# Performance work log

Hardware: AMD Instinct MI355X
Metric: run time of the kernel (lower is better)

The kernel has to match this reference:

```python
import jax, jax.numpy as jnp
import numpy as np

D_MODEL = 512
N_HEADS = 8
HEAD_DIM = D_MODEL // N_HEADS
BATCH = 2
SEQ = 4096
MAX_SEQ = 4096


def _rope_tables(max_len, dim):
    # freqs = 1/10000^(arange(0,dim,2)/dim); outer(t, freqs); polar -> cos/sin
    inv = 1.0 / (10000.0 ** (np.arange(0, dim, 2, dtype=np.float32) / dim))
    t = np.arange(max_len, dtype=np.float32)
    ang = np.outer(t, inv)  # [max_len, dim/2]
    return jnp.asarray(np.cos(ang)), jnp.asarray(np.sin(ang))


def _apply_rope(x, cos, sin):
    # x: [B, S, H, Hd]; complex-pair rotation over last dim pairs
    B, S, H, Hd = x.shape
    xr = x.reshape(B, S, H, Hd // 2, 2)
    xe, xo = xr[..., 0], xr[..., 1]
    c = cos[:S][None, :, None, :]  # [1,S,1,Hd/2]
    s = sin[:S][None, :, None, :]
    re = xe * c - xo * s
    im = xe * s + xo * c
    return jnp.stack([re, im], axis=-1).reshape(B, S, H, Hd)


def setup_inputs() -> dict:
    key = jax.random.key(0)
    kx, kq, kk, kv, ko = jax.random.split(key, 5)
    std = 1.0 / np.sqrt(D_MODEL)
    return {
        "x": jax.random.normal(kx, (BATCH, SEQ, D_MODEL), dtype=jnp.float32),
        "Wq": jax.random.normal(kq, (D_MODEL, D_MODEL), dtype=jnp.float32) * std,
        "Wk": jax.random.normal(kk, (D_MODEL, D_MODEL), dtype=jnp.float32) * std,
        "Wv": jax.random.normal(kv, (D_MODEL, D_MODEL), dtype=jnp.float32) * std,
        "Wo": jax.random.normal(ko, (D_MODEL, D_MODEL), dtype=jnp.float32) * std,
    }


def reference(x, Wq, Wk, Wv, Wo):
    B, S, D = x.shape
    cos, sin = _rope_tables(MAX_SEQ, HEAD_DIM)
    # nn.Linear: y = x @ W.T
    q = (x @ Wq.T).reshape(B, S, N_HEADS, HEAD_DIM)
    k = (x @ Wk.T).reshape(B, S, N_HEADS, HEAD_DIM)
    v = (x @ Wv.T).reshape(B, S, N_HEADS, HEAD_DIM)
    q = _apply_rope(q, cos, sin)
    k = _apply_rope(k, cos, sin)
    scale = HEAD_DIM ** (-0.5)
    # [B,H,S,S]
    scores = jnp.einsum("bshd,bthd->bhst", q, k) * scale
    causal = jnp.tril(jnp.ones((S, S), dtype=bool))
    scores = jnp.where(causal[None, None], scores, -jnp.inf)
    attn = jax.nn.softmax(scores, axis=-1)
    out = jnp.einsum("bhst,bthd->bshd", attn, v).reshape(B, S, D)
    return out @ Wo.T
```

## Files before the change

### kernel.cpp

```cpp
#include <hip/hip_runtime.h>
#include <hip/hip_bf16.h>
#include <math.h>

#define D_MODEL 512
#define N_HEADS 8
#define HEAD_DIM 64
#define BATCH 2
#define SEQ 4096
#define M_ROWS (BATCH*SEQ)

typedef __attribute__((ext_vector_type(8))) short short8;
typedef __attribute__((ext_vector_type(4))) float f32x4;

__device__ inline short f2bf(float f) {
  union { float f; unsigned u; } v; v.f = f;
  unsigned u = v.u;
  unsigned r = u + 0x7FFFu + ((u >> 16) & 1u);
  return (short)(r >> 16);
}
__device__ inline float bf2f(short s) {
  union { unsigned u; float f; } v; v.u = ((unsigned)(unsigned short)s) << 16;
  return v.f;
}

__device__ inline void gll16(const void* g, void* l) {
  __builtin_amdgcn_global_load_lds(
      (const __attribute__((address_space(1))) unsigned int*)g,
      (__attribute__((address_space(3))) unsigned int*)l, 16, 0, 0);
}

__global__ void prep_kernel(const float* __restrict__ x,
                            const float* __restrict__ Wq,
                            const float* __restrict__ Wk,
                            const float* __restrict__ Wv,
                            const float* __restrict__ Wo,
                            short* __restrict__ xb,
                            short* __restrict__ Wqkv,
                            short* __restrict__ Wob,
                            float* __restrict__ cosT,
                            float* __restrict__ sinT) {
  int i = blockIdx.x * blockDim.x + threadIdx.x;
  if (i < M_ROWS * D_MODEL) xb[i] = f2bf(x[i]);
  if (i < 3 * D_MODEL * D_MODEL) {
    int t = i >> 18;
    int r = i & 262143;
    const float* W = (t == 0) ? Wq : ((t == 1) ? Wk : Wv);
    Wqkv[i] = f2bf(W[r]);
  }
  if (i < D_MODEL * D_MODEL) Wob[i] = f2bf(Wo[i]);
  if (i < SEQ * 32) {
    int s = i >> 5, p = i & 31;
    float e = (float)(2 * p) * (1.0f / 64.0f);
    float inv = powf(10000.0f, -e);
    float ang = (float)s * inv;
    float sv, cv;
    sincosf(ang, &sv, &cv);
    cosT[i] = cv; sinT[i] = sv;
  }
}

template<int MODE>
__global__ __launch_bounds__(256) void gemm_kernel(const short* __restrict__ A,
                                                   const short* __restrict__ B,
                                                   float* __restrict__ out_f,
                                                   short* __restrict__ Qb,
                                                   short* __restrict__ Kb,
                                                   short* __restrict__ Vb,
                                                   const float* __restrict__ cosT,
                                                   const float* __restrict__ sinT) {
  __shared__ short smem[128 * 72 * 2];
  short (*As)[72] = (short(*)[72])smem;
  short (*Bs)[72] = (short(*)[72])(smem + 128 * 72);
  short (*Cs)[136] = (short(*)[136])smem;

  const int m0 = blockIdx.x * 128;
  const int n0 = blockIdx.y * 128;
  const int tid = threadIdx.x;
  const int lane = tid & 63, wid = tid >> 6;
  const int wm = wid >> 1, wn = wid & 1;
  const int l15 = lane & 15, g = lane >> 4;
  const int Kdim = 512;

  f32x4 acc[4][4] = {};

  for (int kt = 0; kt < Kdim; kt += 64) {
    __syncthreads();
    for (int it = 0; it < 4; ++it) {
      int c = it * 256 + tid;
      int row = c >> 3, col = (c & 7) << 3;
      *(short8*)&As[row][col] = *(const short8*)&A[(m0 + row) * Kdim + kt + col];
      *(short8*)&Bs[row][col] = *(const short8*)&B[(n0 + row) * Kdim + kt + col];
    }
    __syncthreads();
    for (int kk = 0; kk < 64; kk += 32) {
      short8 a[4], b[4];
      for (int mi = 0; mi < 4; ++mi)
        a[mi] = *(const short8*)&As[wm * 64 + mi * 16 + l15][kk + (g << 3)];
      for (int ni = 0; ni < 4; ++ni)
        b[ni] = *(const short8*)&Bs[wn * 64 + ni * 16 + l15][kk + (g << 3)];
      for (int mi = 0; mi < 4; ++mi)
        for (int ni = 0; ni < 4; ++ni)
          acc[mi][ni] = __builtin_amdgcn_mfma_f32_16x16x32_bf16(a[mi], b[ni], acc[mi][ni], 0, 0, 0);
    }
  }

  if (MODE == 1) {
    for (int mi = 0; mi < 4; ++mi)
      for (int ni = 0; ni < 4; ++ni)
        for (int r = 0; r < 4; ++r) {
          int row_g = m0 + wm * 64 + mi * 16 + (g << 2) + r;
          int col_g = n0 + wn * 64 + ni * 16 + l15;
          out_f[row_g * 512 + col_g] = acc[mi][ni][r];
        }
    return;
  }

  __syncthreads();
  for (int mi = 0; mi < 4; ++mi)
    for (int ni = 0; ni < 4; ++ni)
      for (int r = 0; r < 4; ++r)
        Cs[wm * 64 + mi * 16 + (g << 2) + r][wn * 64 + ni * 16 + l15] =
            f2bf(acc[mi][ni][r]);
  __syncthreads();

  const int t_blk = n0 >> 9;
  if (t_blk < 2) {
    short* dst = (t_blk == 0) ? Qb : Kb;
    const float qs = (t_blk == 0) ? 0.18033688011112042f : 1.0f;
#pragma unroll
    for (int it = 0; it < 8; ++it) {
      int row = (tid >> 4) + (it << 4);
      int colb = (tid & 15) << 3;
      short8 vv = *(const short8*)&Cs[row][colb];
      int row_g = m0 + row;
      int ss = row_g & 4095, bb = row_g >> 12;
      int cc = (n0 + colb) & 511;
      int h = cc >> 6, d = cc & 63;
      int p0 = d >> 1;
      float4 cv = *(const float4*)&cosT[ss * 32 + p0];
      float4 sv = *(const float4*)&sinT[ss * 32 + p0];
      short8 o8;
#pragma unroll
      for (int pp = 0; pp < 4; ++pp) {
        float xe = bf2f(vv[2 * pp]), xo = bf2f(vv[2 * pp + 1]);
        float c = ((const float*)&cv)[pp], s = ((const float*)&sv)[pp];
        o8[2 * pp]     = f2bf((xe * c - xo * s) * qs);
        o8[2 * pp + 1] = f2bf((xe * s + xo * c) * qs);
      }
      *(short8*)&dst[(((bb << 3) + h) * SEQ + ss) * 64 + d] = o8;
    }
  } else {
#pragma unroll
    for (int it = 0; it < 8; ++it) {
      int c = tid & 127;
      int sb = ((tid >> 7) << 3) + (it << 4);
      short8 o8;
#pragma unroll
      for (int j = 0; j < 8; ++j) o8[j] = Cs[sb + j][c];
      int row_g0 = m0 + sb;
      int ss = row_g0 & 4095, bb = row_g0 >> 12;
      int cc = (n0 + c) & 511;
      int h = cc >> 6, d = cc & 63;
      *(short8*)&Vb[((long)(((bb << 3) + h) * 64 + d)) * SEQ + ss] = o8;
    }
  }
}

__global__ __launch_bounds__(512, 2) void attn_kernel(const short* __restrict__ Q,
                                                      const short* __restrict__ K,
                                                      const short* __restrict__ Vt,
                                                      short* __restrict__ O) {
  __shared__ short Ks[2][64 * 64];
  __shared__ short Vs[2][64 * 64];
  __shared__ short P_lds[8][16][72];

  const int lb = blockIdx.x;
  const int bh = ((lb & 7) << 1) + ((lb >> 3) & 1);
  const int pr_ = lb >> 4;
  const int tA = 16 + pr_, tB = 15 - pr_;

  const int tid = threadIdx.x, lane = tid & 63, w = tid >> 6;
  const int l15 = lane & 15, g = lane >> 4;
  const long base = (long)bh * SEQ * 64;
  const long baseV = (long)bh * 64 * SEQ;
  const int bb = bh >> 3, h = bh & 7;

  const int srow = tid >> 3;
  const int sc16k = (tid & 7) ^ (srow & 7);
  short* ldsSegK0 = &Ks[0][(tid >> 6) << 9];
  short* ldsSegK1 = &Ks[1][(tid >> 6) << 9];
  short* ldsSegV0 = &Vs[0][(tid >> 6) << 9];
  short* ldsSegV1 = &Vs[1][(tid >> 6) << 9];

#pragma unroll
  for (int ti = 0; ti < 2; ++ti) {
    const int tile = ti ? tB : tA;
    const int q0 = (tile << 7) + (w << 4);
    const int nc = 2 * tile + 2;

    short8 aq0 = *(const short8*)&Q[base + (long)(q0 + l15) * 64 + (g << 3)];
    short8 aq1 = *(const short8*)&Q[base + (long)(q0 + l15) * 64 + 32 + (g << 3)];

    f32x4 o_acc[4] = {};
    float m_r[4], l_r[4];
#pragma unroll
    for (int r = 0; r < 4; ++r) { m_r[r] = -__builtin_inff(); l_r[r] = 0.f; }

    __syncthreads();
    gll16(&K[base + (long)srow * 64 + sc16k * 8], ldsSegK0);
    gll16(&Vt[baseV + (long)srow * SEQ + sc16k * 8], ldsSegV0);

    for (int c = 0; c < nc; ++c) {
      const int kv0 = c << 6;
      const int bi = c & 1;
      __syncthreads();
      if (c + 1 < nc) {
        const int nkv = (c + 1) << 6;
        short* dK = (bi ? ldsSegK0 : ldsSegK1);
        short* dV = (bi ? ldsSegV0 : ldsSegV1);
        gll16(&K[base + (long)(nkv + srow) * 64 + sc16k * 8], dK);
        gll16(&Vt[baseV + (long)srow * SEQ + nkv + sc16k * 8], dV);
      }
      if (kv0 > q0) continue;

      f32x4 sf[4] = {};
#pragma unroll
      for (int f = 0; f < 4; ++f) {
        int row = f * 16 + l15, sw = row & 7;
        short8 bk0 = *(const short8*)&Ks[bi][row * 64 + ((g) ^ sw) * 8];
        short8 bk1 = *(const short8*)&Ks[bi][row * 64 + ((4 + g) ^ sw) * 8];
        sf[f] = __builtin_amdgcn_mfma_f32_16x16x32_bf16(aq0, bk0, sf[f], 0, 0, 0);
        sf[f] = __builtin_amdgcn_mfma_f32_16x16x32_bf16(aq1, bk1, sf[f], 0, 0, 0);
      }
      if (kv0 == (q0 & ~63)) {
#pragma unroll
        for (int f = 0; f < 4; ++f) {
          int kvc = kv0 + f * 16 + l15;
#pragma unroll
          for (int r = 0; r < 4; ++r) {
            int qrow = q0 + (g << 2) + r;
            if (kvc > qrow) sf[f][r] = -__builtin_inff();
          }
        }
      }

      float pm[4];
#pragma unroll
      for (int r = 0; r < 4; ++r)
        pm[r] = fmaxf(fmaxf(sf[0][r], sf[1][r]), fmaxf(sf[2][r], sf[3][r]));
#pragma unroll
      for (int off = 1; off < 16; off <<= 1)
#pragma unroll
        for (int r = 0; r < 4; ++r)
          pm[r] = fmaxf(pm[r], __shfl_xor(pm[r], off));

      float pr[4][4], rs[4];
#pragma unroll
      for (int r = 0; r < 4; ++r) {
        float mn = fmaxf(m_r[r], pm[r]);
        float alpha = exp2f(m_r[r] - mn);
        m_r[r] = mn;
        l_r[r] *= alpha;
        float s0 = 0.f;
#pragma unroll
        for (int f = 0; f < 4; ++f) {
          float pv = exp2f(sf[f][r] - mn);
          pr[f][r] = pv;
          s0 += pv;
        }
        rs[r] = s0;
#pragma unroll
        for (int db = 0; db < 4; ++db) o_acc[db][r] *= alpha;
      }
#pragma unroll
      for (int off = 1; off < 16; off <<= 1)
#pragma unroll
        for (int r = 0; r < 4; ++r)
          rs[r] += __shfl_xor(rs[r], off);
#pragma unroll
      for (int r = 0; r < 4; ++r) l_r[r] += rs[r];

#pragma unroll
      for (int f = 0; f < 4; ++f)
#pragma unroll
        for (int r = 0; r < 4; ++r)
          P_lds[w][(g << 2) + r][f * 16 + l15] = f2bf(pr[f][r]);

      short8 pa0 = *(const short8*)&P_lds[w][l15][(g << 3)];
      short8 pa1 = *(const short8*)&P_lds[w][l15][32 + (g << 3)];

#pragma unroll
      for (int kk = 0; kk < 2; ++kk) {
        short8 pa = kk ? pa1 : pa0;
#pragma unroll
        for (int db = 0; db < 4; ++db) {
          int row = db * 16 + l15, sw = row & 7;
          short8 bv = *(const short8*)&Vs[bi][row * 64 + ((kk * 4 + g) ^ sw) * 8];
          o_acc[db] = __builtin_amdgcn_mfma_f32_16x16x32_bf16(pa, bv, o_acc[db], 0, 0, 0);
        }
      }
    }

#pragma unroll
    for (int db = 0; db < 4; ++db)
#pragma unroll
      for (int r = 0; r < 4; ++r) {
        int s_g = q0 + (g << 2) + r;
        float v = o_acc[db][r] / l_r[r];
        O[((long)(bb * SEQ + s_g)) * 512 + h * 64 + db * 16 + l15] = f2bf(v);
      }
  }
}

extern "C" void kernel_launch(void* const* d_in, const int* in_sizes, int n_in,
                              void* d_out, int out_size, void* d_ws, size_t ws_size,
                              hipStream_t stream) {
  const float* x  = (const float*)d_in[0];
  const float* Wq = (const float*)d_in[1];
  const float* Wk = (const float*)d_in[2];
  const float* Wv = (const float*)d_in[3];
  const float* Wo = (const float*)d_in[4];

  char* ws = (char*)d_ws;
  size_t off = 0;
  auto alloc = [&](size_t bytes) {
    void* p = ws + off;
    off += (bytes + 255) & ~(size_t)255;
    return p;
  };
  short* xb   = (short*)alloc((size_t)M_ROWS * 512 * 2);
  short* Wqkv = (short*)alloc((size_t)1536 * 512 * 2);
  short* Wob  = (short*)alloc((size_t)512 * 512 * 2);
  float* cosT = (float*)alloc((size_t)SEQ * 32 * 4);
  float* sinT = (float*)alloc((size_t)SEQ * 32 * 4);
  short* Qb   = (short*)alloc((size_t)16 * SEQ * 64 * 2);
  short* Kb   = (short*)alloc((size_t)16 * SEQ * 64 * 2);
  short* Vt   = (short*)alloc((size_t)16 * SEQ * 64 * 2);
  short* Obuf = (short*)alloc((size_t)M_ROWS * 512 * 2);

  prep_kernel<<<16384, 256, 0, stream>>>(x, Wq, Wk, Wv, Wo, xb, Wqkv, Wob, cosT, sinT);
  gemm_kernel<0><<<dim3(64, 12), 256, 0, stream>>>(xb, Wqkv, nullptr, Qb, Kb, Vt, cosT, sinT);
  attn_kernel<<<256, 512, 0, stream>>>(Qb, Kb, Vt, Obuf);
  gemm_kernel<1><<<dim3(64, 4), 256, 0, stream>>>(Obuf, Wob, (float*)d_out, nullptr, nullptr, nullptr, nullptr, nullptr);
}
```

Measured before the change: 246.8 us.

## Split attention into one tile per block, apply RoPE in fp32 before bf16 store

The attention kernel now launches 512 blocks with one query tile each, ordered longest first, in place of 256 blocks that each processed a paired long and short tile. Launch bounds are raised to 4 blocks per CU, and s_setprio is raised around the MFMA sections. In the QKV GEMM epilogue, RoPE and the Q scale are applied to the fp32 accumulators using a lane shuffle for the pair partner, before rounding to bf16. This removes the bf16 round trip and the float4 cos/sin loads in the store loop, at the cost of scalar table loads per element. More blocks may improve load balance and latency hiding but lose the work pairing, and tighter launch bounds may cause register spills.

Result: slower. 252.5 us (+2.3%).

```diff
diff --git a/kernel.cpp b/kernel.cpp
--- a/kernel.cpp
+++ b/kernel.cpp
@@ -115,18 +115,35 @@
     return;
   }
 
+  const int t_blk = n0 >> 9;
   __syncthreads();
-  for (int mi = 0; mi < 4; ++mi)
-    for (int ni = 0; ni < 4; ++ni)
-      for (int r = 0; r < 4; ++r)
-        Cs[wm * 64 + mi * 16 + (g << 2) + r][wn * 64 + ni * 16 + l15] =
-            f2bf(acc[mi][ni][r]);
+
+  if (t_blk < 2) {
+    const float qs = (t_blk == 0) ? 0.18033688011112042f : 1.0f;
+    for (int mi = 0; mi < 4; ++mi)
+      for (int ni = 0; ni < 4; ++ni)
+        for (int r = 0; r < 4; ++r) {
+          int lrow = wm * 64 + mi * 16 + (g << 2) + r;
+          int ss = (m0 + lrow) & 4095;
+          int d = (n0 + wn * 64 + ni * 16 + l15) & 63;
+          int p = d >> 1;
+          float c = cosT[ss * 32 + p], s = sinT[ss * 32 + p];
+          float v = acc[mi][ni][r];
+          float partner = __shfl_xor(v, 1);
+          float res = (l15 & 1) ? (v * c + partner * s) : (v * c - partner * s);
+          Cs[lrow][wn * 64 + ni * 16 + l15] = f2bf(res * qs);
+        }
+  } else {
+    for (int mi = 0; mi < 4; ++mi)
+      for (int ni = 0; ni < 4; ++ni)
+        for (int r = 0; r < 4; ++r)
+          Cs[wm * 64 + mi * 16 + (g << 2) + r][wn * 64 + ni * 16 + l15] =
+              f2bf(acc[mi][ni][r]);
+  }
   __syncthreads();
 
-  const int t_blk = n0 >> 9;
   if (t_blk < 2) {
     short* dst = (t_blk == 0) ? Qb : Kb;
-    const float qs = (t_blk == 0) ? 0.18033688011112042f : 1.0f;
 #pragma unroll
     for (int it = 0; it < 8; ++it) {
       int row = (tid >> 4) + (it << 4);
@@ -136,18 +153,7 @@
       int ss = row_g & 4095, bb = row_g >> 12;
       int cc = (n0 + colb) & 511;
       int h = cc >> 6, d = cc & 63;
-      int p0 = d >> 1;
-      float4 cv = *(const float4*)&cosT[ss * 32 + p0];
-      float4 sv = *(const float4*)&sinT[ss * 32 + p0];
-      short8 o8;
-#pragma unroll
-      for (int pp = 0; pp < 4; ++pp) {
-        float xe = bf2f(vv[2 * pp]), xo = bf2f(vv[2 * pp + 1]);
-        float c = ((const float*)&cv)[pp], s = ((const float*)&sv)[pp];
-        o8[2 * pp]     = f2bf((xe * c - xo * s) * qs);
-        o8[2 * pp + 1] = f2bf((xe * s + xo * c) * qs);
-      }
-      *(short8*)&dst[(((bb << 3) + h) * SEQ + ss) * 64 + d] = o8;
+      *(short8*)&dst[(((bb << 3) + h) * SEQ + ss) * 64 + d] = vv;
     }
   } else {
 #pragma unroll
@@ -166,7 +172,7 @@
   }
 }
 
-__global__ __launch_bounds__(512, 2) void attn_kernel(const short* __restrict__ Q,
+__global__ __launch_bounds__(512, 4) void attn_kernel(const short* __restrict__ Q,
                                                       const short* __restrict__ K,
                                                       const short* __restrict__ Vt,
                                                       short* __restrict__ O) {
@@ -174,10 +180,10 @@
   __shared__ short Vs[2][64 * 64];
   __shared__ short P_lds[8][16][72];
 
-  const int lb = blockIdx.x;
-  const int bh = ((lb & 7) << 1) + ((lb >> 3) & 1);
-  const int pr_ = lb >> 4;
-  const int tA = 16 + pr_, tB = 15 - pr_;
+  const int o = blockIdx.x;
+  const int j = o >> 4;
+  const int bh = o & 15;
+  const int tile = (o < 256) ? (31 - j) : (j - 16);
 
   const int tid = threadIdx.x, lane = tid & 63, w = tid >> 6;
   const int l15 = lane & 15, g = lane >> 4;
@@ -192,124 +198,123 @@
   short* ldsSegV0 = &Vs[0][(tid >> 6) << 9];
   short* ldsSegV1 = &Vs[1][(tid >> 6) << 9];
 
-#pragma unroll
-  for (int ti = 0; ti < 2; ++ti) {
-    const int tile = ti ? tB : tA;
-    const int q0 = (tile << 7) + (w << 4);
-    const int nc = 2 * tile + 2;
-
-    short8 aq0 = *(const short8*)&Q[base + (long)(q0 + l15) * 64 + (g << 3)];
-    short8 aq1 = *(const short8*)&Q[base + (long)(q0 + l15) * 64 + 32 + (g << 3)];
-
-    f32x4 o_acc[4] = {};
-    float m_r[4], l_r[4];
-#pragma unroll
-    for (int r = 0; r < 4; ++r) { m_r[r] = -__builtin_inff(); l_r[r] = 0.f; }
-
+  const int q0 = (tile << 7) + (w << 4);
+  const int nc = 2 * tile + 2;
+
+  short8 aq0 = *(const short8*)&Q[base + (long)(q0 + l15) * 64 + (g << 3)];
+  short8 aq1 = *(const short8*)&Q[base + (long)(q0 + l15) * 64 + 32 + (g << 3)];
+
+  f32x4 o_acc[4] = {};
+  float m_r[4], l_r[4];
+#pragma unroll
+  for (int r = 0; r < 4; ++r) { m_r[r] = -__builtin_inff(); l_r[r] = 0.f; }
+
+  gll16(&K[base + (long)srow * 64 + sc16k * 8], ldsSegK0);
+  gll16(&Vt[baseV + (long)srow * SEQ + sc16k * 8], ldsSegV0);
+
+  for (int c = 0; c < nc; ++c) {
+    const int kv0 = c << 6;
+    const int bi = c & 1;
     __syncthreads();
-    gll16(&K[base + (long)srow * 64 + sc16k * 8], ldsSegK0);
-    gll16(&Vt[baseV + (long)srow * SEQ + sc16k * 8], ldsSegV0);
-
-    for (int c = 0; c < nc; ++c) {
-      const int kv0 = c << 6;
-      const int bi = c & 1;
-      __syncthreads();
-      if (c + 1 < nc) {
-        const int nkv = (c + 1) << 6;
-        short* dK = (bi ? ldsSegK0 : ldsSegK1);
-        short* dV = (bi ? ldsSegV0 : ldsSegV1);
-        gll16(&K[base + (long)(nkv + srow) * 64 + sc16k * 8], dK);
-        gll16(&Vt[baseV + (long)srow * SEQ + nkv + sc16k * 8], dV);
-      }
-      if (kv0 > q0) continue;
-
-      f32x4 sf[4] = {};
+    if (c + 1 < nc) {
+      const int nkv = (c + 1) << 6;
+      short* dK = (bi ? ldsSegK0 : ldsSegK1);
+      short* dV = (bi ? ldsSegV0 : ldsSegV1);
+      gll16(&K[base + (long)(nkv + srow) * 64 + sc16k * 8], dK);
+      gll16(&Vt[baseV + (long)srow * SEQ + nkv + sc16k * 8], dV);
+    }
+    if (kv0 > q0) continue;
+
+    f32x4 sf[4] = {};
+    __builtin_amdgcn_s_setprio(1);
+#pragma unroll
+    for (int f = 0; f < 4; ++f) {
+      int row = f * 16 + l15, sw = row & 7;
+      short8 bk0 = *(const short8*)&Ks[bi][row * 64 + ((g) ^ sw) * 8];
+      short8 bk1 = *(const short8*)&Ks[bi][row * 64 + ((4 + g) ^ sw) * 8];
+      sf[f] = __builtin_amdgcn_mfma_f32_16x16x32_bf16(aq0, bk0, sf[f], 0, 0, 0);
+      sf[f] = __builtin_amdgcn_mfma_f32_16x16x32_bf16(aq1, bk1, sf[f], 0, 0, 0);
+    }
+    __builtin_amdgcn_s_setprio(0);
+    if (kv0 == (q0 & ~63)) {
 #pragma unroll
       for (int f = 0; f < 4; ++f) {
-        int row = f * 16 + l15, sw = row & 7;
-        short8 bk0 = *(const short8*)&Ks[bi][row * 64 + ((g) ^ sw) * 8];
-        short8 bk1 = *(const short8*)&Ks[bi][row * 64 + ((4 + g) ^ sw) * 8];
-        sf[f] = __builtin_amdgcn_mfma_f32_16x16x32_bf16(aq0, bk0, sf[f], 0, 0, 0);
-        sf[f] = __builtin_amdgcn_mfma_f32_16x16x32_bf16(aq1, bk1, sf[f], 0, 0, 0);
-      }
-      if (kv0 == (q0 & ~63)) {
-#pragma unroll
-        for (int f = 0; f < 4; ++f) {
-          int kvc = kv0 + f * 16 + l15;
-#pragma unroll
-          for (int r = 0; r < 4; ++r) {
-            int qrow = q0 + (g << 2) + r;
-            if (kvc > qrow) sf[f][r] = -__builtin_inff();
-          }
+        int kvc = kv0 + f * 16 + l15;
+#pragma unroll
+        for (int r = 0; r < 4; ++r) {
+          int qrow = q0 + (g << 2) + r;
+          if (kvc > qrow) sf[f][r] = -__builtin_inff();
         }
       }
-
-      float pm[4];
+    }
+
+    float pm[4];
+#pragma unroll
+    for (int r = 0; r < 4; ++r)
+      pm[r] = fmaxf(fmaxf(sf[0][r], sf[1][r]), fmaxf(sf[2][r], sf[3][r]));
+#pragma unroll
+    for (int off = 1; off < 16; off <<= 1)
 #pragma unroll
       for (int r = 0; r < 4; ++r)
-        pm[r] = fmaxf(fmaxf(sf[0][r], sf[1][r]), fmaxf(sf[2][r], sf[3][r]));
-#pragma unroll
-      for (int off = 1; off < 16; off <<= 1)
-#pragma unroll
-        for (int r = 0; r < 4; ++r)
-          pm[r] = fmaxf(pm[r], __shfl_xor(pm[r], off));
-
-      float pr[4][4], rs[4];
-#pragma unroll
-      for (int r = 0; r < 4; ++r) {
-        float mn = fmaxf(m_r[r], pm[r]);
-        float alpha = exp2f(m_r[r] - mn);
-        m_r[r] = mn;
-        l_r[r] *= alpha;
-        float s0 = 0.f;
-#pragma unroll
-        for (int f = 0; f < 4; ++f) {
-          float pv = exp2f(sf[f][r] - mn);
-          pr[f][r] = pv;
-          s0 += pv;
-        }
-        rs[r] = s0;
-#pragma unroll
-        for (int db = 0; db < 4; ++db) o_acc[db][r] *= alpha;
+        pm[r] = fmaxf(pm[r], __shfl_xor(pm[r], off));
+
+    float pr[4][4], rs[4];
+#pragma unroll
+    for (int r = 0; r < 4; ++r) {
+      float mn = fmaxf(m_r[r], pm[r]);
+      float alpha = exp2f(m_r[r] - mn);
+      m_r[r] = mn;
+      l_r[r] *= alpha;
+      float s0 = 0.f;
+#pragma unroll
+      for (int f = 0; f < 4; ++f) {
+        float pv = exp2f(sf[f][r] - mn);
+        pr[f][r] = pv;
+        s0 += pv;
       }
-#pragma unroll
-      for (int off = 1; off < 16; off <<= 1)
-#pragma unroll
-        for (int r = 0; r < 4; ++r)
-          rs[r] += __shfl_xor(rs[r], off);
-#pragma unroll
-      for (int r = 0; r < 4; ++r) l_r[r] += rs[r];
-
-#pragma unroll
-      for (int f = 0; f < 4; ++f)
-#pragma unroll
-        for (int r = 0; r < 4; ++r)
-          P_lds[w][(g << 2) + r][f * 16 + l15] = f2bf(pr[f][r]);
-
-      short8 pa0 = *(const short8*)&P_lds[w][l15][(g << 3)];
-      short8 pa1 = *(const short8*)&P_lds[w][l15][32 + (g << 3)];
-
-#pragma unroll
-      for (int kk = 0; kk < 2; ++kk) {
-        short8 pa = kk ? pa1 : pa0;
-#pragma unroll
-        for (int db = 0; db < 4; ++db) {
-          int row = db * 16 + l15, sw = row & 7;
-          short8 bv = *(const short8*)&Vs[bi][row * 64 + ((kk * 4 + g) ^ sw) * 8];
-          o_acc[db] = __builtin_amdgcn_mfma_f32_16x16x32_bf16(pa, bv, o_acc[db], 0, 0, 0);
-        }
+      rs[r] = s0;
+#pragma unroll
+      for (int db = 0; db < 4; ++db) o_acc[db][r] *= alpha;
+    }
+#pragma unroll
+    for (int off = 1; off < 16; off <<= 1)
+#pragma unroll
+      for (int r = 0; r < 4; ++r)
+        rs[r] += __shfl_xor(rs[r], off);
+#pragma unroll
+    for (int r = 0; r < 4; ++r) l_r[r] += rs[r];
+
+#pragma unroll
+    for (int f = 0; f < 4; ++f)
+#pragma unroll
+      for (int r = 0; r < 4; ++r)
+        P_lds[w][(g << 2) + r][f * 16 + l15] = f2bf(pr[f][r]);
+
+    short8 pa0 = *(const short8*)&P_lds[w][l15][(g << 3)];
+    short8 pa1 = *(const short8*)&P_lds[w][l15][32 + (g << 3)];
+
+    __builtin_amdgcn_s_setprio(1);
+#pragma unroll
+    for (int kk = 0; kk < 2; ++kk) {
+      short8 pa = kk ? pa1 : pa0;
+#pragma unroll
+      for (int db = 0; db < 4; ++db) {
+        int row = db * 16 + l15, sw = row & 7;
+        short8 bv = *(const short8*)&Vs[bi][row * 64 + ((kk * 4 + g) ^ sw) * 8];
+        o_acc[db] = __builtin_amdgcn_mfma_f32_16x16x32_bf16(pa, bv, o_acc[db], 0, 0, 0);
       }
     }
-
-#pragma unroll
-    for (int db = 0; db < 4; ++db)
-#pragma unroll
-      for (int r = 0; r < 4; ++r) {
-        int s_g = q0 + (g << 2) + r;
-        float v = o_acc[db][r] / l_r[r];
-        O[((long)(bb * SEQ + s_g)) * 512 + h * 64 + db * 16 + l15] = f2bf(v);
-      }
-  }
+    __builtin_amdgcn_s_setprio(0);
+  }
+
+#pragma unroll
+  for (int db = 0; db < 4; ++db)
+#pragma unroll
+    for (int r = 0; r < 4; ++r) {
+      int s_g = q0 + (g << 2) + r;
+      float v = o_acc[db][r] / l_r[r];
+      O[((long)(bb * SEQ + s_g)) * 512 + h * 64 + db * 16 + l15] = f2bf(v);
+    }
 }
 
 extern "C" void kernel_launch(void* const* d_in, const int* in_sizes, int n_in,
@@ -340,6 +345,6 @@
 
   prep_kernel<<<16384, 256, 0, stream>>>(x, Wq, Wk, Wv, Wo, xb, Wqkv, Wob, cosT, sinT);
   gemm_kernel<0><<<dim3(64, 12), 256, 0, stream>>>(xb, Wqkv, nullptr, Qb, Kb, Vt, cosT, sinT);
-  attn_kernel<<<256, 512, 0, stream>>>(Qb, Kb, Vt, Obuf);
+  attn_kernel<<<512, 512, 0, stream>>>(Qb, Kb, Vt, Obuf);
   gemm_kernel<1><<<dim3(64, 4), 256, 0, stream>>>(Obuf, Wob, (float*)d_out, nullptr, nullptr, nullptr, nullptr, nullptr);
 }
```
